# Performance work log

Hardware: AMD Instinct MI355X
Metric: run time of the kernel (lower is better)

The kernel has to match this reference:

```python
import jax, jax.numpy as jnp
import numpy as np

N = 100000      # num_nodes
E = 400000      # num edges
HID = 128       # hidden_channels (== in_channels, memory dim)
OUT = 64        # out_channels (per head)
HEADS = 4
HD = HEADS * OUT  # 256, TransformerConv concat output dim


def _lin(k, fan_in, fan_out):
    return jax.random.normal(k, (fan_in, fan_out), jnp.float32) * 0.02


def setup_inputs() -> dict:
    key = jax.random.key(0)
    ks = jax.random.split(key, 16)
    return {
        "edge_index": jax.random.randint(ks[0], (2, E), 0, N, dtype=jnp.int64),
        "edge_time": jax.random.randint(ks[1], (E, 1), 0, 1000000, dtype=jnp.int64),
        "x": jax.random.normal(ks[2], (N, HID), jnp.float32),
        "memory": jax.random.normal(ks[3], (N, HID), jnp.float32),  # TGN memory table (detached in fwd)
        # TransformerConv params (lin_query / lin_key / lin_value / lin_skip, all with bias)
        "Wq": _lin(ks[4], HID, HD), "bq": jnp.zeros((HD,), jnp.float32),
        "Wk": _lin(ks[5], HID, HD), "bk": jnp.zeros((HD,), jnp.float32),
        "Wv": _lin(ks[6], HID, HD), "bv": jnp.zeros((HD,), jnp.float32),
        "Wskip": _lin(ks[7], HID, HD), "bskip": jnp.zeros((HD,), jnp.float32),
        # rating MLP: Linear(512,128) -> ReLU -> Linear(128,64) -> ReLU -> Linear(64,1)
        "W1": _lin(ks[8], 2 * HD, 128), "b1": jnp.zeros((128,), jnp.float32),
        "W2": _lin(ks[9], 128, 64), "b2": jnp.zeros((64,), jnp.float32),
        "W3": _lin(ks[10], 64, 1), "b3": jnp.zeros((1,), jnp.float32),
    }


def reference(edge_index, edge_time, x, memory,
              Wq, bq, Wk, bk, Wv, bv, Wskip, bskip,
              W1, b1, W2, b2, W3, b3):
    src, dst = edge_index[0], edge_index[1]
    n = x.shape[0]

    # x = memory.detach() + x
    h = memory + x  # [N, HID]

    # TransformerConv (heads=4, concat=True, root_weight=True)
    q = (h @ Wq + bq).reshape(n, HEADS, OUT)
    k = (h @ Wk + bk).reshape(n, HEADS, OUT)
    v = (h @ Wv + bv).reshape(n, HEADS, OUT)

    # per-edge attention scores: messages flow src -> dst, softmax over in-edges of dst
    scores = jnp.sum(q[dst] * k[src], axis=-1) / jnp.sqrt(jnp.float32(OUT))  # [E, H]
    smax = jax.ops.segment_max(scores, dst, num_segments=n)                   # [N, H]
    e = jnp.exp(scores - smax[dst])
    denom = jax.ops.segment_sum(e, dst, num_segments=n)
    alpha = e / (denom[dst] + 1e-16)                                          # [E, H]

    agg = jax.ops.segment_sum(alpha[:, :, None] * v[src], dst, num_segments=n)  # [N, H, OUT]
    out = agg.reshape(n, HD) + (h @ Wskip + bskip)                              # skip connection

    # interaction embeddings + MLP head (dropout inactive at eval)
    inter = jnp.concatenate([out[src], out[dst]], axis=-1)  # [E, 512]
    hdd = jax.nn.relu(inter @ W1 + b1)
    hdd = jax.nn.relu(hdd @ W2 + b2)
    rating = jax.nn.sigmoid(hdd @ W3 + b3) * 4.0 + 1.0
    return rating[:, 0]
```

## Files before the change

### kernel.cpp

```cpp
#include <hip/hip_runtime.h>
#include <math.h>

#define N_NODES 100000
#define N_EDGES 400000
#define HID 128
#define HEADS 4
#define OUT_C 64
#define HD 256
#define SCAN_CHUNK 1024
#define NB_SCAN ((N_NODES + SCAN_CHUNK - 1) / SCAN_CHUNK)
#define SLAB_STRIDE 4356
#define PSLAB_W 2576

typedef __attribute__((ext_vector_type(8))) short bf16x8;
typedef __attribute__((ext_vector_type(4))) float f32x4;

__device__ __forceinline__ unsigned short fbf(float f) {
    unsigned u = __float_as_uint(f);
    unsigned r = (u + 0x7fffu + ((u >> 16) & 1u)) >> 16;
    return (unsigned short)r;
}
__device__ __forceinline__ float bf2f(unsigned short u) {
    return __uint_as_float(((unsigned)u) << 16);
}

__device__ __forceinline__ void gl_lds16(const void* g, void* l) {
    __builtin_amdgcn_global_load_lds(
        (const __attribute__((address_space(1))) unsigned int*)g,
        (__attribute__((address_space(3))) unsigned int*)l,
        16, 0, 0);
}

__global__ __launch_bounds__(256) void k_deg(const int* __restrict__ ei,
                                             int* __restrict__ deg) {
    int e = blockIdx.x * 256 + threadIdx.x;
    if (e < N_EDGES) atomicAdd(&deg[ei[N_EDGES + e]], 1);
}

__global__ __launch_bounds__(256) void k_scan1(const int* __restrict__ deg,
                                               int* __restrict__ rp,
                                               int* __restrict__ bsum) {
    __shared__ int ts[256];
    int b = blockIdx.x, t = threadIdx.x;
    int base = b * SCAN_CHUNK + t * 4;
    int vv[4];
    int s = 0;
#pragma unroll
    for (int i = 0; i < 4; ++i) {
        int d = (base + i < N_NODES) ? deg[base + i] : 0;
        vv[i] = s;
        s += d;
    }
    ts[t] = s;
    __syncthreads();
    for (int off = 1; off < 256; off <<= 1) {
        int x = (t >= off) ? ts[t - off] : 0;
        __syncthreads();
        ts[t] += x;
        __syncthreads();
    }
    int ex = ts[t] - s;
#pragma unroll
    for (int i = 0; i < 4; ++i)
        if (base + i < N_NODES) rp[base + i] = ex + vv[i];
    if (t == 255) bsum[b] = ts[255];
}

__global__ __launch_bounds__(256) void k_scan2(int* __restrict__ bsum) {
    __shared__ int ts[256];
    int t = threadIdx.x;
    int v = (t < NB_SCAN) ? bsum[t] : 0;
    ts[t] = v;
    __syncthreads();
    for (int off = 1; off < 256; off <<= 1) {
        int x = (t >= off) ? ts[t - off] : 0;
        __syncthreads();
        ts[t] += x;
        __syncthreads();
    }
    if (t < NB_SCAN) bsum[t] = ts[t] - v;
}

__global__ __launch_bounds__(256) void k_bucket(const int* __restrict__ ei,
                                                const int* __restrict__ rp,
                                                const int* __restrict__ bsum,
                                                int* __restrict__ cursor,
                                                int* __restrict__ csr_src,
                                                int* __restrict__ csr_dst,
                                                int* __restrict__ csr_eid) {
    int e = blockIdx.x * 256 + threadIdx.x;
    if (e >= N_EDGES) return;
    int src = ei[e];
    int d   = ei[N_EDGES + e];
    int idx = atomicAdd(&cursor[d], 1);
    int s   = rp[d] + bsum[d >> 10] + idx;
    csr_src[s] = src;
    csr_dst[s] = d;
    csr_eid[s] = e;
}

__global__ __launch_bounds__(256) void pack_all(
    const float* __restrict__ Wq, const float* __restrict__ Wk,
    const float* __restrict__ Wv, const float* __restrict__ Ws,
    const float* __restrict__ W1, const float* __restrict__ W2,
    unsigned short* __restrict__ Wp, unsigned short* __restrict__ Wcp,
    unsigned short* __restrict__ W2p) {
    int i = blockIdx.x * 256 + threadIdx.x;
    int lane = i & 63;
    int q = lane >> 4, c = lane & 15;
    if (i < 16384) {
        int nt = (i >> 6) & 15, kt = (i >> 10) & 3, z = i >> 12;
        const float* W = (z == 0) ? Wq : (z == 1) ? Wk : (z == 2) ? Wv : Ws;
#pragma unroll
        for (int j = 0; j < 8; ++j)
            Wp[i * 8 + j] = fbf(W[(kt * 32 + q * 8 + j) * HD + nt * 16 + c]);
    } else if (i < 24576) {
        int ii = i - 16384;
        int nt = (ii >> 6) & 15, kt = ii >> 10;
        int n = nt * 16 + c;
#pragma unroll
        for (int j = 0; j < 8; ++j) {
            int k = kt * 32 + q * 8 + j;
            float v = (n < 128) ? W1[k * 128 + n] : W1[(k + 256) * 128 + (n - 128)];
            Wcp[ii * 8 + j] = fbf(v);
        }
    } else if (i < 25600) {
        int ii = i - 24576;
        int nt = (ii >> 6) & 3, kt = ii >> 8;
#pragma unroll
        for (int j = 0; j < 8; ++j)
            W2p[ii * 8 + j] = fbf(W2[(kt * 32 + q * 8 + j) * 64 + nt * 16 + c]);
    }
}

__global__ __launch_bounds__(256) void k_pre(const float* __restrict__ x,
                                             const float* __restrict__ mem,
                                             unsigned short* __restrict__ H) {
    int idx = blockIdx.x * 256 + threadIdx.x;
    if (idx >= N_NODES * HID / 8) return;
    const float4* x4 = (const float4*)x;
    const float4* m4 = (const float4*)mem;
    float4 a0 = x4[(size_t)idx * 2],     a1 = x4[(size_t)idx * 2 + 1];
    float4 b0 = m4[(size_t)idx * 2],     b1 = m4[(size_t)idx * 2 + 1];
    bf16x8 hv;
    hv[0] = (short)fbf(a0.x + b0.x); hv[1] = (short)fbf(a0.y + b0.y);
    hv[2] = (short)fbf(a0.z + b0.z); hv[3] = (short)fbf(a0.w + b0.w);
    hv[4] = (short)fbf(a1.x + b1.x); hv[5] = (short)fbf(a1.y + b1.y);
    hv[6] = (short)fbf(a1.z + b1.z); hv[7] = (short)fbf(a1.w + b1.w);
    *(bf16x8*)&H[(size_t)idx * 8] = hv;
}

__device__ __forceinline__ void mfma_pass(f32x4 acc[4][4], const short* As,
        const unsigned short* __restrict__ Wp, int z, int w, int l, int q, int c) {
#pragma unroll
    for (int mt = 0; mt < 4; ++mt)
#pragma unroll
        for (int nt = 0; nt < 4; ++nt) acc[mt][nt] = (f32x4){0.f, 0.f, 0.f, 0.f};
#pragma unroll
    for (int kt = 0; kt < 4; ++kt) {
        bf16x8 af[4];
#pragma unroll
        for (int mt = 0; mt < 4; ++mt) {
            int row  = mt * 16 + c;
            int slot = (kt * 4 + q) ^ (row & 7);
            af[mt] = *(const bf16x8*)&As[row * 128 + slot * 8];
        }
#pragma unroll
        for (int nt = 0; nt < 4; ++nt) {
            bf16x8 bw8 = *(const bf16x8*)&Wp[(size_t)(((z * 4 + kt) * 16 + w * 4 + nt) * 64 + l) * 8];
#pragma unroll
            for (int mt = 0; mt < 4; ++mt)
                acc[mt][nt] = __builtin_amdgcn_mfma_f32_16x16x32_bf16(af[mt], bw8, acc[mt][nt], 0, 0, 0);
        }
    }
}

__device__ __forceinline__ void slab_store(short* slab, const f32x4 acc[4][4],
        const float bb[4], int q, int c) {
#pragma unroll
    for (int nt = 0; nt < 4; ++nt)
#pragma unroll
        for (int mt = 0; mt < 4; ++mt)
#pragma unroll
            for (int r = 0; r < 4; ++r)
                slab[(mt * 16 + q * 4 + r) * 68 + nt * 16 + c] =
                    (short)fbf(acc[mt][nt][r] + bb[nt]);
}

__device__ __forceinline__ void store_rows(unsigned short* __restrict__ O,
        const short* slab, int m0, int w, int l) {
    const int srow = l >> 3, schk = l & 7;
#pragma unroll
    for (int j = 0; j < 8; ++j) {
        int row = j * 8 + srow;
        int gr  = m0 + row;
        if (gr < N_NODES)
            *(bf16x8*)&O[(size_t)gr * HD + w * 64 + schk * 8] =
                *(const bf16x8*)&slab[row * 68 + schk * 8];
    }
}

__global__ __launch_bounds__(256, 3) void gemm4(
    const unsigned short* __restrict__ H,
    const unsigned short* __restrict__ Wp,
    const float* __restrict__ bq, const float* __restrict__ bk,
    const float* __restrict__ bv, const float* __restrict__ bs,
    unsigned short* __restrict__ Q, unsigned short* __restrict__ KV,
    unsigned short* __restrict__ S)
{
    __shared__ __align__(16) short As[64 * 128];
    __shared__ __align__(16) short Slab[4 * SLAB_STRIDE];

    const int t = threadIdx.x;
    const int w = t >> 6, l = t & 63;
    const int q = l >> 4, c = l & 15;
    const int y  = blockIdx.y;
    const int m0 = blockIdx.x * 64;

#pragma unroll
    for (int i = 0; i < 4; ++i) {
        int rbase = w * 16 + i * 4;
        int r  = rbase + (l >> 4);
        int gr = m0 + r; if (gr >= N_NODES) gr = N_NODES - 1;
        int ks = (l & 15) ^ (r & 7);
        gl_lds16(&H[(size_t)gr * HID + ks * 8], &As[rbase * 128]);
    }

    const int   zA  = (y == 0) ? 0 : 1;
    const int   zB  = (y == 0) ? 3 : 2;
    const float* bA = (y == 0) ? bq : bk;
    const float* bB = (y == 0) ? bs : bv;
    float bbA[4], bbB[4];
#pragma unroll
    for (int nt = 0; nt < 4; ++nt) {
        bbA[nt] = bA[w * 64 + nt * 16 + c];
        bbB[nt] = bB[w * 64 + nt * 16 + c];
    }

    __syncthreads();

    short* slab = &Slab[w * SLAB_STRIDE];
    f32x4 acc[4][4];
    ushort4 kreg[16];
    const int koff = (l & 15) * 4;
    const short* cslab = &Slab[(l >> 4) * SLAB_STRIDE];

    mfma_pass(acc, As, Wp, zA, w, l, q, c);
    slab_store(slab, acc, bbA, q, c);
    if (y == 0) {
        store_rows(Q, slab, m0, w, l);
    } else {
        __syncthreads();
#pragma unroll
        for (int i = 0; i < 16; ++i)
            kreg[i] = *(const ushort4*)&cslab[(w * 16 + i) * 68 + koff];
        __syncthreads();
    }

    mfma_pass(acc, As, Wp, zB, w, l, q, c);
    slab_store(slab, acc, bbB, q, c);
    if (y == 0) {
        store_rows(S, slab, m0, w, l);
    } else {
        __syncthreads();
#pragma unroll
        for (int i = 0; i < 16; ++i) {
            int gr = m0 + w * 16 + i;
            ushort4 vr = *(const ushort4*)&cslab[(w * 16 + i) * 68 + koff];
            if (gr < N_NODES) {
                bf16x8 ov;
                ov[0] = (short)kreg[i].x; ov[1] = (short)kreg[i].y;
                ov[2] = (short)kreg[i].z; ov[3] = (short)kreg[i].w;
                ov[4] = (short)vr.x;      ov[5] = (short)vr.y;
                ov[6] = (short)vr.z;      ov[7] = (short)vr.w;
                *(bf16x8*)&KV[(size_t)gr * 512 + l * 8] = ov;
            }
        }
    }
}

__global__ __launch_bounds__(512, 6) void attn_pd(
    const int* __restrict__ rp, const int* __restrict__ bsum,
    const int* __restrict__ deg, const int* __restrict__ csr_src,
    const unsigned short* __restrict__ Q, const unsigned short* __restrict__ KV,
    const unsigned short* __restrict__ S,
    const unsigned short* __restrict__ Wcp,
    unsigned short* __restrict__ PD)
{
    __shared__ __align__(16) short sh[8 * PSLAB_W];
    short* As = sh;

    const int t = threadIdx.x;
    const int w = t >> 6, l = t & 63;
    const int q = l >> 4, c = l & 15;
    const int m0 = blockIdx.x * 64;

    int meta = 0;
    {
        int nn = m0 + w * 8 + (l & 7);
        if (nn < N_NODES) {
            if (l < 8)       meta = rp[nn] + bsum[nn >> 10];
            else if (l < 16) meta = deg[nn];
        }
    }

    for (int i = 0; i < 8; ++i) {
        int row  = w * 8 + i;
        int node = m0 + row;
        if (node < N_NODES) {
            int start = __shfl(meta, i);
            int cnt   = __shfl(meta, 8 + i);

            float q0, q1, q2, q3;
            ushort4 su;
            {
                ushort4 u = *(const ushort4*)&Q[(size_t)node * HD + l * 4];
                su = *(const ushort4*)&S[(size_t)node * HD + l * 4];
                q0 = bf2f(u.x) * 0.125f; q1 = bf2f(u.y) * 0.125f;
                q2 = bf2f(u.z) * 0.125f; q3 = bf2f(u.w) * 0.125f;
            }

            float d = 0.f;
            float a0 = 0.f, a1 = 0.f, a2 = 0.f, a3 = 0.f;

            int i2 = 0;
            for (; i2 + 4 <= cnt; i2 += 4) {
                int s0 = csr_src[start + i2];
                int s1 = csr_src[start + i2 + 1];
                int s2 = csr_src[start + i2 + 2];
                int s3 = csr_src[start + i2 + 3];
                bf16x8 k0 = *(const bf16x8*)&KV[(size_t)s0 * 512 + l * 8];
                bf16x8 k1 = *(const bf16x8*)&KV[(size_t)s1 * 512 + l * 8];
                bf16x8 k2 = *(const bf16x8*)&KV[(size_t)s2 * 512 + l * 8];
                bf16x8 k3 = *(const bf16x8*)&KV[(size_t)s3 * 512 + l * 8];
                float sA = q0 * bf2f((unsigned short)k0[0]) + q1 * bf2f((unsigned short)k0[1])
                         + q2 * bf2f((unsigned short)k0[2]) + q3 * bf2f((unsigned short)k0[3]);
                float sB = q0 * bf2f((unsigned short)k1[0]) + q1 * bf2f((unsigned short)k1[1])
                         + q2 * bf2f((unsigned short)k1[2]) + q3 * bf2f((unsigned short)k1[3]);
                float sC = q0 * bf2f((unsigned short)k2[0]) + q1 * bf2f((unsigned short)k2[1])
                         + q2 * bf2f((unsigned short)k2[2]) + q3 * bf2f((unsigned short)k2[3]);
                float sD = q0 * bf2f((unsigned short)k3[0]) + q1 * bf2f((unsigned short)k3[1])
                         + q2 * bf2f((unsigned short)k3[2]) + q3 * bf2f((unsigned short)k3[3]);
                sA += __shfl_xor(sA, 1); sB += __shfl_xor(sB, 1);
                sC += __shfl_xor(sC, 1); sD += __shfl_xor(sD, 1);
                sA += __shfl_xor(sA, 2); sB += __shfl_xor(sB, 2);
                sC += __shfl_xor(sC, 2); sD += __shfl_xor(sD, 2);
                sA += __shfl_xor(sA, 4); sB += __shfl_xor(sB, 4);
                sC += __shfl_xor(sC, 4); sD += __shfl_xor(sD, 4);
                sA += __shfl_xor(sA, 8); sB += __shfl_xor(sB, 8);
                sC += __shfl_xor(sC, 8); sD += __shfl_xor(sD, 8);
                float eA = __expf(sA), eB = __expf(sB), eC = __expf(sC), eD = __expf(sD);
                d += (eA + eB) + (eC + eD);
                a0 += eA * bf2f((unsigned short)k0[4]) + eB * bf2f((unsigned short)k1[4])
                    + eC * bf2f((unsigned short)k2[4]) + eD * bf2f((unsigned short)k3[4]);
                a1 += eA * bf2f((unsigned short)k0[5]) + eB * bf2f((unsigned short)k1[5])
                    + eC * bf2f((unsigned short)k2[5]) + eD * bf2f((unsigned short)k3[5]);
                a2 += eA * bf2f((unsigned short)k0[6]) + eB * bf2f((unsigned short)k1[6])
                    + eC * bf2f((unsigned short)k2[6]) + eD * bf2f((unsigned short)k3[6]);
                a3 += eA * bf2f((unsigned short)k0[7]) + eB * bf2f((unsigned short)k1[7])
                    + eC * bf2f((unsigned short)k2[7]) + eD * bf2f((unsigned short)k3[7]);
            }
            if (i2 + 2 <= cnt) {
                int s0 = csr_src[start + i2];
                int s1 = csr_src[start + i2 + 1];
                bf16x8 k0 = *(const bf16x8*)&KV[(size_t)s0 * 512 + l * 8];
                bf16x8 k1 = *(const bf16x8*)&KV[(size_t)s1 * 512 + l * 8];
                float sA = q0 * bf2f((unsigned short)k0[0]) + q1 * bf2f((unsigned short)k0[1])
                         + q2 * bf2f((unsigned short)k0[2]) + q3 * bf2f((unsigned short)k0[3]);
                float sB = q0 * bf2f((unsigned short)k1[0]) + q1 * bf2f((unsigned short)k1[1])
                         + q2 * bf2f((unsigned short)k1[2]) + q3 * bf2f((unsigned short)k1[3]);
                sA += __shfl_xor(sA, 1); sB += __shfl_xor(sB, 1);
                sA += __shfl_xor(sA, 2); sB += __shfl_xor(sB, 2);
                sA += __shfl_xor(sA, 4); sB += __shfl_xor(sB, 4);
                sA += __shfl_xor(sA, 8); sB += __shfl_xor(sB, 8);
                float eA = __expf(sA), eB = __expf(sB);
                d += eA + eB;
                a0 += eA * bf2f((unsigned short)k0[4]) + eB * bf2f((unsigned short)k1[4]);
                a1 += eA * bf2f((unsigned short)k0[5]) + eB * bf2f((unsigned short)k1[5]);
                a2 += eA * bf2f((unsigned short)k0[6]) + eB * bf2f((unsigned short)k1[6]);
                a3 += eA * bf2f((unsigned short)k0[7]) + eB * bf2f((unsigned short)k1[7]);
                i2 += 2;
            }
            if (i2 < cnt) {
                int s0 = csr_src[start + i2];
                bf16x8 k0 = *(const bf16x8*)&KV[(size_t)s0 * 512 + l * 8];
                float sA = q0 * bf2f((unsigned short)k0[0]) + q1 * bf2f((unsigned short)k0[1])
                         + q2 * bf2f((unsigned short)k0[2]) + q3 * bf2f((unsigned short)k0[3]);
                sA += __shfl_xor(sA, 1);
                sA += __shfl_xor(sA, 2);
                sA += __shfl_xor(sA, 4);
                sA += __shfl_xor(sA, 8);
                float eA = __expf(sA);
                d += eA;
                a0 += eA * bf2f((unsigned short)k0[4]);
                a1 += eA * bf2f((unsigned short)k0[5]);
                a2 += eA * bf2f((unsigned short)k0[6]);
                a3 += eA * bf2f((unsigned short)k0[7]);
            }

            float inv = 1.f / (d + 1e-16f);
            ushort4 ov = make_ushort4(fbf(bf2f(su.x) + a0 * inv),
                                      fbf(bf2f(su.y) + a1 * inv),
                                      fbf(bf2f(su.z) + a2 * inv),
                                      fbf(bf2f(su.w) + a3 * inv));
            *(ushort4*)&As[row * 256 + (((l >> 1) ^ (row & 7)) << 3) + ((l & 1) << 2)] = ov;
        }
    }
    __syncthreads();

    f32x4 acc[4][2];
#pragma unroll
    for (int mt = 0; mt < 4; ++mt)
#pragma unroll
        for (int nt = 0; nt < 2; ++nt) acc[mt][nt] = (f32x4){0.f, 0.f, 0.f, 0.f};

#pragma unroll
    for (int kt = 0; kt < 8; ++kt) {
        bf16x8 af[4];
#pragma unroll
        for (int mt = 0; mt < 4; ++mt) {
            int row  = mt * 16 + c;
            int slot = (kt * 4 + q) ^ (row & 7);
            af[mt] = *(const bf16x8*)&As[row * 256 + slot * 8];
        }
#pragma unroll
        for (int nt = 0; nt < 2; ++nt) {
            int ntg = w * 2 + nt;
            bf16x8 bv8 = *(const bf16x8*)&Wcp[(size_t)((kt * 16 + ntg) * 64 + l) * 8];
#pragma unroll
            for (int mt = 0; mt < 4; ++mt)
                acc[mt][nt] = __builtin_amdgcn_mfma_f32_16x16x32_bf16(af[mt], bv8, acc[mt][nt], 0, 0, 0);
        }
    }
    __syncthreads();

    short* slab = &sh[w * PSLAB_W];
#pragma unroll
    for (int nt = 0; nt < 2; ++nt)
#pragma unroll
        for (int mt = 0; mt < 4; ++mt)
#pragma unroll
            for (int r = 0; r < 4; ++r)
                slab[(mt * 16 + q * 4 + r) * 40 + nt * 16 + c] =
                    (short)fbf(acc[mt][nt][r]);
    __syncthreads();

    const int cc = l & 31;
    const short* sb = &sh[(cc >> 2) * PSLAB_W + (cc & 3) * 8];
#pragma unroll
    for (int i = 0; i < 4; ++i) {
        int row = w * 8 + i * 2 + (l >> 5);
        int gr  = m0 + row;
        if (gr < N_NODES)
            *(bf16x8*)&PD[(size_t)gr * HD + cc * 8] = *(const bf16x8*)&sb[row * 40];
    }
}

__global__ __launch_bounds__(256) void edge_mlp_pd(
    const int* __restrict__ csr_src, const int* __restrict__ csr_dst,
    const int* __restrict__ csr_eid,
    const unsigned short* __restrict__ PD,
    const float* __restrict__ b1,
    const unsigned short* __restrict__ W2p, const float* __restrict__ b2,
    const float* __restrict__ W3, const float* __restrict__ b3,
    float* __restrict__ rating)
{
    __shared__ __align__(16) char lds[64 * 136 * 2];
    short* h1t = (short*)lds;
    float* h2s = (float*)lds;

    const int t = threadIdx.x;
    const int w = t >> 6, l = t & 63;
    const int q = l >> 4, c = l & 15;
    const int e0 = blockIdx.x * 64;

#pragma unroll
    for (int j = 0; j < 4; ++j) {
        int idx = t + j * 256;
        int row = idx >> 4, ch = idx & 15;
        int src = csr_src[e0 + row];
        int dst = csr_dst[e0 + row];
        bf16x8 pv = *(const bf16x8*)&PD[(size_t)src * HD + ch * 8];
        bf16x8 dv = *(const bf16x8*)&PD[(size_t)dst * HD + 128 + ch * 8];
        float4 ba = *(const float4*)&b1[ch * 8];
        float4 bb = *(const float4*)&b1[ch * 8 + 4];
        bf16x8 hv;
        hv[0] = (short)fbf(fmaxf(bf2f((unsigned short)pv[0]) + bf2f((unsigned short)dv[0]) + ba.x, 0.f));
        hv[1] = (short)fbf(fmaxf(bf2f((unsigned short)pv[1]) + bf2f((unsigned short)dv[1]) + ba.y, 0.f));
        hv[2] = (short)fbf(fmaxf(bf2f((unsigned short)pv[2]) + bf2f((unsigned short)dv[2]) + ba.z, 0.f));
        hv[3] = (short)fbf(fmaxf(bf2f((unsigned short)pv[3]) + bf2f((unsigned short)dv[3]) + ba.w, 0.f));
        hv[4] = (short)fbf(fmaxf(bf2f((unsigned short)pv[4]) + bf2f((unsigned short)dv[4]) + bb.x, 0.f));
        hv[5] = (short)fbf(fmaxf(bf2f((unsigned short)pv[5]) + bf2f((unsigned short)dv[5]) + bb.y, 0.f));
        hv[6] = (short)fbf(fmaxf(bf2f((unsigned short)pv[6]) + bf2f((unsigned short)dv[6]) + bb.z, 0.f));
        hv[7] = (short)fbf(fmaxf(bf2f((unsigned short)pv[7]) + bf2f((unsigned short)dv[7]) + bb.w, 0.f));
        *(bf16x8*)&h1t[row * 136 + ch * 8] = hv;
    }
    __syncthreads();

    f32x4 acc2[4];
#pragma unroll
    for (int i = 0; i < 4; ++i) acc2[i] = (f32x4){0.f, 0.f, 0.f, 0.f};
#pragma unroll
    for (int kt = 0; kt < 4; ++kt) {
        bf16x8 av = *(const bf16x8*)&h1t[(w * 16 + c) * 136 + kt * 32 + q * 8];
#pragma unroll
        for (int nt = 0; nt < 4; ++nt) {
            bf16x8 bv = *(const bf16x8*)&W2p[(size_t)((kt * 4 + nt) * 64 + l) * 8];
            acc2[nt] = __builtin_amdgcn_mfma_f32_16x16x32_bf16(av, bv, acc2[nt], 0, 0, 0);
        }
    }
    __syncthreads();

#pragma unroll
    for (int nt = 0; nt < 4; ++nt) {
        float bv = b2[nt * 16 + c];
#pragma unroll
        for (int r = 0; r < 4; ++r)
            h2s[(w * 16 + q * 4 + r) * 65 + nt * 16 + c] = fmaxf(acc2[nt][r] + bv, 0.f);
    }
    __syncthreads();

    {
        int e = t >> 2, part = t & 3;
        float a = 0.f;
#pragma unroll
        for (int kk = 0; kk < 16; ++kk)
            a += h2s[e * 65 + part * 16 + kk] * W3[part * 16 + kk];
        a += __shfl_xor(a, 1);
        a += __shfl_xor(a, 2);
        if (part == 0)
            rating[csr_eid[e0 + e]] = 4.f / (1.f + __expf(-(a + b3[0]))) + 1.f;
    }
}

extern "C" void kernel_launch(void* const* d_in, const int* in_sizes, int n_in,
                              void* d_out, int out_size, void* d_ws, size_t ws_size,
                              hipStream_t stream) {
    const int*   ei  = (const int*)d_in[0];
    const float* x   = (const float*)d_in[2];
    const float* mem = (const float*)d_in[3];
    const float* Wq  = (const float*)d_in[4];
    const float* bq  = (const float*)d_in[5];
    const float* Wk  = (const float*)d_in[6];
    const float* bk  = (const float*)d_in[7];
    const float* Wv  = (const float*)d_in[8];
    const float* bv  = (const float*)d_in[9];
    const float* Ws  = (const float*)d_in[10];
    const float* bs  = (const float*)d_in[11];
    const float* W1  = (const float*)d_in[12];
    const float* b1  = (const float*)d_in[13];
    const float* W2  = (const float*)d_in[14];
    const float* b2  = (const float*)d_in[15];
    const float* W3  = (const float*)d_in[16];
    const float* b3  = (const float*)d_in[17];
    float* rating = (float*)d_out;

    unsigned short* Q = (unsigned short*)d_ws;
    const size_t NHDe = (size_t)N_NODES * HD;
    unsigned short* KV = Q + NHDe;
    unsigned short* S  = KV + 2 * NHDe;
    unsigned short* H  = S + NHDe;
    int* rp      = (int*)(H + (size_t)N_NODES * HID);
    int* deg     = rp + N_NODES;
    int* cursor  = deg + N_NODES;
    int* csr_src = cursor + N_NODES;
    int* csr_dst = csr_src + N_EDGES;
    int* csr_eid = csr_dst + N_EDGES;
    int* bsum    = csr_eid + N_EDGES;
    unsigned short* Wp  = (unsigned short*)(bsum + 128);
    unsigned short* Wcp = Wp + 16384 * 8;
    unsigned short* W2p = Wcp + 8192 * 8;
    unsigned short* PD  = Q;

    const int eblk  = (N_EDGES + 255) / 256;
    const int pblk  = (N_NODES * HID / 8 + 255) / 256;
    const int gblk  = (N_NODES + 63) / 64;

    hipMemsetAsync(deg, 0, sizeof(int) * 2 * N_NODES, stream);
    k_deg<<<eblk, 256, 0, stream>>>(ei, deg);
    k_scan1<<<NB_SCAN, 256, 0, stream>>>(deg, rp, bsum);
    k_scan2<<<1, 256, 0, stream>>>(bsum);
    k_bucket<<<eblk, 256, 0, stream>>>(ei, rp, bsum, cursor, csr_src, csr_dst, csr_eid);
    pack_all<<<100, 256, 0, stream>>>(Wq, Wk, Wv, Ws, W1, W2, Wp, Wcp, W2p);

    k_pre<<<pblk, 256, 0, stream>>>(x, mem, H);

    gemm4<<<dim3(gblk, 2), dim3(256), 0, stream>>>(
        H, Wp, bq, bk, bv, bs, Q, KV, S);

    attn_pd<<<gblk, 512, 0, stream>>>(rp, bsum, deg, csr_src, Q, KV, S, Wcp, PD);

    edge_mlp_pd<<<N_EDGES / 64, 256, 0, stream>>>(
        csr_src, csr_dst, csr_eid, PD, b1, W2p, b2, W3, b3, rating);
}
```

Measured before the change: 416.2 us.

## Split projection GEMM into QS and KV kernels with transposed MFMA direct stores

The combined gemm4 kernel is replaced by two 512-thread kernels, one producing Q and skip and one producing interleaved K/V. Each computes a transposed product (weights times H) so every lane owns four consecutive output columns and can write them straight to global memory, which drops the LDS slab staging and the extra barriers. attn_pd's output epilogue now reuses a smaller LDS region in two halves so its launch bound can rise to 8 blocks. The aim is less LDS traffic and higher occupancy, at the cost of an extra kernel launch and less coalesced global stores.

After: 598.4 us. 43.8% more time.

```diff
diff --git a/kernel.cpp b/kernel.cpp
--- a/kernel.cpp
+++ b/kernel.cpp
@@ -9,8 +9,7 @@
 #define HD 256
 #define SCAN_CHUNK 1024
 #define NB_SCAN ((N_NODES + SCAN_CHUNK - 1) / SCAN_CHUNK)
-#define SLAB_STRIDE 4356
-#define PSLAB_W 2576
+#define PSLAB 2576
 
 typedef __attribute__((ext_vector_type(8))) short bf16x8;
 typedef __attribute__((ext_vector_type(4))) float f32x4;
@@ -150,136 +149,176 @@
     *(bf16x8*)&H[(size_t)idx * 8] = hv;
 }
 
-__device__ __forceinline__ void mfma_pass(f32x4 acc[4][4], const short* As,
-        const unsigned short* __restrict__ Wp, int z, int w, int l, int q, int c) {
-#pragma unroll
-    for (int mt = 0; mt < 4; ++mt)
-#pragma unroll
-        for (int nt = 0; nt < 4; ++nt) acc[mt][nt] = (f32x4){0.f, 0.f, 0.f, 0.f};
-#pragma unroll
-    for (int kt = 0; kt < 4; ++kt) {
-        bf16x8 af[4];
-#pragma unroll
-        for (int mt = 0; mt < 4; ++mt) {
-            int row  = mt * 16 + c;
-            int slot = (kt * 4 + q) ^ (row & 7);
-            af[mt] = *(const bf16x8*)&As[row * 128 + slot * 8];
-        }
-#pragma unroll
-        for (int nt = 0; nt < 4; ++nt) {
-            bf16x8 bw8 = *(const bf16x8*)&Wp[(size_t)(((z * 4 + kt) * 16 + w * 4 + nt) * 64 + l) * 8];
-#pragma unroll
-            for (int mt = 0; mt < 4; ++mt)
-                acc[mt][nt] = __builtin_amdgcn_mfma_f32_16x16x32_bf16(af[mt], bw8, acc[mt][nt], 0, 0, 0);
-        }
-    }
-}
-
-__device__ __forceinline__ void slab_store(short* slab, const f32x4 acc[4][4],
-        const float bb[4], int q, int c) {
-#pragma unroll
-    for (int nt = 0; nt < 4; ++nt)
-#pragma unroll
-        for (int mt = 0; mt < 4; ++mt)
-#pragma unroll
-            for (int r = 0; r < 4; ++r)
-                slab[(mt * 16 + q * 4 + r) * 68 + nt * 16 + c] =
-                    (short)fbf(acc[mt][nt][r] + bb[nt]);
-}
-
-__device__ __forceinline__ void store_rows(unsigned short* __restrict__ O,
-        const short* slab, int m0, int w, int l) {
-    const int srow = l >> 3, schk = l & 7;
-#pragma unroll
-    for (int j = 0; j < 8; ++j) {
-        int row = j * 8 + srow;
-        int gr  = m0 + row;
-        if (gr < N_NODES)
-            *(bf16x8*)&O[(size_t)gr * HD + w * 64 + schk * 8] =
-                *(const bf16x8*)&slab[row * 68 + schk * 8];
-    }
-}
-
-__global__ __launch_bounds__(256, 3) void gemm4(
-    const unsigned short* __restrict__ H,
-    const unsigned short* __restrict__ Wp,
-    const float* __restrict__ bq, const float* __restrict__ bk,
-    const float* __restrict__ bv, const float* __restrict__ bs,
-    unsigned short* __restrict__ Q, unsigned short* __restrict__ KV,
-    unsigned short* __restrict__ S)
-{
-    __shared__ __align__(16) short As[64 * 128];
-    __shared__ __align__(16) short Slab[4 * SLAB_STRIDE];
-
-    const int t = threadIdx.x;
-    const int w = t >> 6, l = t & 63;
-    const int q = l >> 4, c = l & 15;
-    const int y  = blockIdx.y;
-    const int m0 = blockIdx.x * 64;
-
-#pragma unroll
-    for (int i = 0; i < 4; ++i) {
-        int rbase = w * 16 + i * 4;
+__device__ __forceinline__ void stage_h(const unsigned short* __restrict__ H,
+                                        short* As, int m0, int w, int l) {
+#pragma unroll
+    for (int i = 0; i < 2; ++i) {
+        int rbase = w * 8 + i * 4;
         int r  = rbase + (l >> 4);
         int gr = m0 + r; if (gr >= N_NODES) gr = N_NODES - 1;
         int ks = (l & 15) ^ (r & 7);
         gl_lds16(&H[(size_t)gr * HID + ks * 8], &As[rbase * 128]);
     }
-
-    const int   zA  = (y == 0) ? 0 : 1;
-    const int   zB  = (y == 0) ? 3 : 2;
-    const float* bA = (y == 0) ? bq : bk;
-    const float* bB = (y == 0) ? bs : bv;
-    float bbA[4], bbB[4];
-#pragma unroll
-    for (int nt = 0; nt < 4; ++nt) {
-        bbA[nt] = bA[w * 64 + nt * 16 + c];
-        bbB[nt] = bB[w * 64 + nt * 16 + c];
-    }
-
-    __syncthreads();
-
-    short* slab = &Slab[w * SLAB_STRIDE];
-    f32x4 acc[4][4];
-    ushort4 kreg[16];
-    const int koff = (l & 15) * 4;
-    const short* cslab = &Slab[(l >> 4) * SLAB_STRIDE];
-
-    mfma_pass(acc, As, Wp, zA, w, l, q, c);
-    slab_store(slab, acc, bbA, q, c);
-    if (y == 0) {
-        store_rows(Q, slab, m0, w, l);
-    } else {
-        __syncthreads();
-#pragma unroll
-        for (int i = 0; i < 16; ++i)
-            kreg[i] = *(const ushort4*)&cslab[(w * 16 + i) * 68 + koff];
-        __syncthreads();
-    }
-
-    mfma_pass(acc, As, Wp, zB, w, l, q, c);
-    slab_store(slab, acc, bbB, q, c);
-    if (y == 0) {
-        store_rows(S, slab, m0, w, l);
-    } else {
-        __syncthreads();
-#pragma unroll
-        for (int i = 0; i < 16; ++i) {
-            int gr = m0 + w * 16 + i;
-            ushort4 vr = *(const ushort4*)&cslab[(w * 16 + i) * 68 + koff];
-            if (gr < N_NODES) {
+}
+
+__global__ __launch_bounds__(512, 6) void gemm_qs(
+    const unsigned short* __restrict__ H,
+    const unsigned short* __restrict__ Wp,
+    const float* __restrict__ bq, const float* __restrict__ bs,
+    unsigned short* __restrict__ Q, unsigned short* __restrict__ S)
+{
+    __shared__ __align__(16) short As[64 * 128];
+
+    const int t = threadIdx.x;
+    const int w = t >> 6, l = t & 63;
+    const int q = l >> 4, c = l & 15;
+    const int m0 = blockIdx.x * 64;
+
+    stage_h(H, As, m0, w, l);
+    __syncthreads();
+
+#pragma unroll
+    for (int zz = 0; zz < 2; ++zz) {
+        const int z = (zz == 0) ? 0 : 3;
+        const float* bz = (zz == 0) ? bq : bs;
+        unsigned short* Oz = (zz == 0) ? Q : S;
+
+        f32x4 acc[2][4];
+#pragma unroll
+        for (int mt = 0; mt < 2; ++mt)
+#pragma unroll
+            for (int nt = 0; nt < 4; ++nt) acc[mt][nt] = (f32x4){0.f, 0.f, 0.f, 0.f};
+
+#pragma unroll
+        for (int kt = 0; kt < 4; ++kt) {
+            bf16x8 hf[4];
+#pragma unroll
+            for (int nt = 0; nt < 4; ++nt) {
+                int row  = nt * 16 + c;
+                int slot = (kt * 4 + q) ^ (row & 7);
+                hf[nt] = *(const bf16x8*)&As[row * 128 + slot * 8];
+            }
+#pragma unroll
+            for (int mt = 0; mt < 2; ++mt) {
+                bf16x8 wf = *(const bf16x8*)&Wp[(size_t)(((z * 4 + kt) * 16 + w * 2 + mt) * 64 + l) * 8];
+#pragma unroll
+                for (int nt = 0; nt < 4; ++nt)
+                    acc[mt][nt] = __builtin_amdgcn_mfma_f32_16x16x32_bf16(wf, hf[nt], acc[mt][nt], 0, 0, 0);
+            }
+        }
+
+#pragma unroll
+        for (int mt = 0; mt < 2; ++mt) {
+            float4 bb = *(const float4*)&bz[w * 32 + mt * 16 + q * 4];
+#pragma unroll
+            for (int nt = 0; nt < 4; ++nt) {
+                int node = m0 + nt * 16 + c;
+                if (node < N_NODES) {
+                    ushort4 ov = make_ushort4(fbf(acc[mt][nt][0] + bb.x),
+                                              fbf(acc[mt][nt][1] + bb.y),
+                                              fbf(acc[mt][nt][2] + bb.z),
+                                              fbf(acc[mt][nt][3] + bb.w));
+                    *(ushort4*)&Oz[(size_t)node * HD + w * 32 + mt * 16 + q * 4] = ov;
+                }
+            }
+        }
+    }
+}
+
+__global__ __launch_bounds__(512, 6) void gemm_kv(
+    const unsigned short* __restrict__ H,
+    const unsigned short* __restrict__ Wp,
+    const float* __restrict__ bk, const float* __restrict__ bv,
+    unsigned short* __restrict__ KV)
+{
+    __shared__ __align__(16) short As[64 * 128];
+
+    const int t = threadIdx.x;
+    const int w = t >> 6, l = t & 63;
+    const int q = l >> 4, c = l & 15;
+    const int m0 = blockIdx.x * 64;
+
+    stage_h(H, As, m0, w, l);
+    __syncthreads();
+
+    f32x4 acc[2][4];
+    ushort4 kf[2][4];
+
+#pragma unroll
+    for (int mt = 0; mt < 2; ++mt)
+#pragma unroll
+        for (int nt = 0; nt < 4; ++nt) acc[mt][nt] = (f32x4){0.f, 0.f, 0.f, 0.f};
+#pragma unroll
+    for (int kt = 0; kt < 4; ++kt) {
+        bf16x8 hf[4];
+#pragma unroll
+        for (int nt = 0; nt < 4; ++nt) {
+            int row  = nt * 16 + c;
+            int slot = (kt * 4 + q) ^ (row & 7);
+            hf[nt] = *(const bf16x8*)&As[row * 128 + slot * 8];
+        }
+#pragma unroll
+        for (int mt = 0; mt < 2; ++mt) {
+            bf16x8 wf = *(const bf16x8*)&Wp[(size_t)(((1 * 4 + kt) * 16 + w * 2 + mt) * 64 + l) * 8];
+#pragma unroll
+            for (int nt = 0; nt < 4; ++nt)
+                acc[mt][nt] = __builtin_amdgcn_mfma_f32_16x16x32_bf16(wf, hf[nt], acc[mt][nt], 0, 0, 0);
+        }
+    }
+#pragma unroll
+    for (int mt = 0; mt < 2; ++mt) {
+        float4 bb = *(const float4*)&bk[w * 32 + mt * 16 + q * 4];
+#pragma unroll
+        for (int nt = 0; nt < 4; ++nt)
+            kf[mt][nt] = make_ushort4(fbf(acc[mt][nt][0] + bb.x),
+                                      fbf(acc[mt][nt][1] + bb.y),
+                                      fbf(acc[mt][nt][2] + bb.z),
+                                      fbf(acc[mt][nt][3] + bb.w));
+    }
+
+#pragma unroll
+    for (int mt = 0; mt < 2; ++mt)
+#pragma unroll
+        for (int nt = 0; nt < 4; ++nt) acc[mt][nt] = (f32x4){0.f, 0.f, 0.f, 0.f};
+#pragma unroll
+    for (int kt = 0; kt < 4; ++kt) {
+        bf16x8 hf[4];
+#pragma unroll
+        for (int nt = 0; nt < 4; ++nt) {
+            int row  = nt * 16 + c;
+            int slot = (kt * 4 + q) ^ (row & 7);
+            hf[nt] = *(const bf16x8*)&As[row * 128 + slot * 8];
+        }
+#pragma unroll
+        for (int mt = 0; mt < 2; ++mt) {
+            bf16x8 wf = *(const bf16x8*)&Wp[(size_t)(((2 * 4 + kt) * 16 + w * 2 + mt) * 64 + l) * 8];
+#pragma unroll
+            for (int nt = 0; nt < 4; ++nt)
+                acc[mt][nt] = __builtin_amdgcn_mfma_f32_16x16x32_bf16(wf, hf[nt], acc[mt][nt], 0, 0, 0);
+        }
+    }
+
+#pragma unroll
+    for (int mt = 0; mt < 2; ++mt) {
+        float4 bb = *(const float4*)&bv[w * 32 + mt * 16 + q * 4];
+#pragma unroll
+        for (int nt = 0; nt < 4; ++nt) {
+            int node = m0 + nt * 16 + c;
+            if (node < N_NODES) {
                 bf16x8 ov;
-                ov[0] = (short)kreg[i].x; ov[1] = (short)kreg[i].y;
-                ov[2] = (short)kreg[i].z; ov[3] = (short)kreg[i].w;
-                ov[4] = (short)vr.x;      ov[5] = (short)vr.y;
-                ov[6] = (short)vr.z;      ov[7] = (short)vr.w;
-                *(bf16x8*)&KV[(size_t)gr * 512 + l * 8] = ov;
-            }
-        }
-    }
-}
-
-__global__ __launch_bounds__(512, 6) void attn_pd(
+                ov[0] = (short)kf[mt][nt].x; ov[1] = (short)kf[mt][nt].y;
+                ov[2] = (short)kf[mt][nt].z; ov[3] = (short)kf[mt][nt].w;
+                ov[4] = (short)fbf(acc[mt][nt][0] + bb.x);
+                ov[5] = (short)fbf(acc[mt][nt][1] + bb.y);
+                ov[6] = (short)fbf(acc[mt][nt][2] + bb.z);
+                ov[7] = (short)fbf(acc[mt][nt][3] + bb.w);
+                *(bf16x8*)&KV[(size_t)node * 512 + (w * 8 + mt * 4 + q) * 8] = ov;
+            }
+        }
+    }
+}
+
+__global__ __launch_bounds__(512, 8) void attn_pd(
     const int* __restrict__ rp, const int* __restrict__ bsum,
     const int* __restrict__ deg, const int* __restrict__ csr_src,
     const unsigned short* __restrict__ Q, const unsigned short* __restrict__ KV,
@@ -287,7 +326,7 @@
     const unsigned short* __restrict__ Wcp,
     unsigned short* __restrict__ PD)
 {
-    __shared__ __align__(16) short sh[8 * PSLAB_W];
+    __shared__ __align__(16) short sh[64 * 256];
     short* As = sh;
 
     const int t = threadIdx.x;
@@ -434,25 +473,34 @@
     }
     __syncthreads();
 
-    short* slab = &sh[w * PSLAB_W];
-#pragma unroll
-    for (int nt = 0; nt < 2; ++nt)
-#pragma unroll
-        for (int mt = 0; mt < 4; ++mt)
-#pragma unroll
-            for (int r = 0; r < 4; ++r)
-                slab[(mt * 16 + q * 4 + r) * 40 + nt * 16 + c] =
-                    (short)fbf(acc[mt][nt][r]);
-    __syncthreads();
-
-    const int cc = l & 31;
-    const short* sb = &sh[(cc >> 2) * PSLAB_W + (cc & 3) * 8];
-#pragma unroll
-    for (int i = 0; i < 4; ++i) {
-        int row = w * 8 + i * 2 + (l >> 5);
-        int gr  = m0 + row;
-        if (gr < N_NODES)
-            *(bf16x8*)&PD[(size_t)gr * HD + cc * 8] = *(const bf16x8*)&sb[row * 40];
+#pragma unroll
+    for (int h = 0; h < 2; ++h) {
+        if ((w >> 2) == h) {
+            short* slab = &sh[(w & 3) * PSLAB];
+#pragma unroll
+            for (int nt = 0; nt < 2; ++nt)
+#pragma unroll
+                for (int mt = 0; mt < 4; ++mt)
+#pragma unroll
+                    for (int r = 0; r < 4; ++r)
+                        slab[(mt * 16 + q * 4 + r) * 40 + nt * 16 + c] =
+                            (short)fbf(acc[mt][nt][r]);
+        }
+        __syncthreads();
+        {
+            int cl   = l & 15;
+            int rsub = l >> 4;
+            const short* sb = &sh[(cl >> 2) * PSLAB + (cl & 3) * 8];
+#pragma unroll
+            for (int i = 0; i < 2; ++i) {
+                int row = w * 8 + i * 4 + rsub;
+                int gr  = m0 + row;
+                if (gr < N_NODES)
+                    *(bf16x8*)&PD[(size_t)gr * HD + (h * 16 + cl) * 8] =
+                        *(const bf16x8*)&sb[row * 40];
+            }
+        }
+        __syncthreads();
     }
 }
 
@@ -585,8 +633,8 @@
 
     k_pre<<<pblk, 256, 0, stream>>>(x, mem, H);
 
-    gemm4<<<dim3(gblk, 2), dim3(256), 0, stream>>>(
-        H, Wp, bq, bk, bv, bs, Q, KV, S);
+    gemm_qs<<<gblk, 512, 0, stream>>>(H, Wp, bq, bs, Q, S);
+    gemm_kv<<<gblk, 512, 0, stream>>>(H, Wp, bk, bv, KV);
 
     attn_pd<<<gblk, 512, 0, stream>>>(rp, bsum, deg, csr_src, Q, KV, S, Wcp, PD);
 
```
